# Kernel optimization log

Measured on AMD Instinct MI355X. Metric: run time of the kernel, lower is better.

## Reference

```python
import jax, jax.numpy as jnp
import numpy as np

IOU_THRESHOLD = 0.5
NEG_POS_RATIO = 3
FOCAL_ALPHA = 0.25
FOCAL_GAMMA = 2.0
LOC_LOSS_WEIGHT = 1.0
EPS = 1e-7


def _make_boxes(key, shape):
    # valid xyxy boxes in [0,1]
    k1, k2 = jax.random.split(key)
    xy1 = jax.random.uniform(k1, shape[:-1] + (2,)) * 0.8
    wh = jax.random.uniform(k2, shape[:-1] + (2,)) * 0.2 + 0.01
    return jnp.concatenate([xy1, xy1 + wh], axis=-1)


def setup_inputs() -> dict:
    key = jax.random.key(0)
    k1, k2, k3 = jax.random.split(key, 3)
    B, A, G = 16, 65536, 64
    bbox_pred = _make_boxes(k1, (B, A, 4))
    conf_pred = jax.random.normal(k2, (B, A), dtype=jnp.float32)
    gt_boxes = _make_boxes(k3, (B, G, 4))
    return {"bbox_pred": bbox_pred, "conf_pred": conf_pred, "gt_boxes": gt_boxes}


def box_iou(a, b):
    # a: [A,4], b: [G,4] xyxy -> [A,G]
    area_a = (a[:, 2] - a[:, 0]) * (a[:, 3] - a[:, 1])
    area_b = (b[:, 2] - b[:, 0]) * (b[:, 3] - b[:, 1])
    lt = jnp.maximum(a[:, None, :2], b[None, :, :2])
    rb = jnp.minimum(a[:, None, 2:], b[None, :, 2:])
    wh = jnp.clip(rb - lt, 0.0)
    inter = wh[..., 0] * wh[..., 1]
    return inter / (area_a[:, None] + area_b[None, :] - inter + EPS)


def diou_loss(pred, gt):
    # pred, gt: [N,4] xyxy -> [N]
    area_p = (pred[:, 2] - pred[:, 0]) * (pred[:, 3] - pred[:, 1])
    area_g = (gt[:, 2] - gt[:, 0]) * (gt[:, 3] - gt[:, 1])
    lt = jnp.maximum(pred[:, :2], gt[:, :2])
    rb = jnp.minimum(pred[:, 2:], gt[:, 2:])
    wh = jnp.clip(rb - lt, 0.0)
    inter = wh[:, 0] * wh[:, 1]
    iou = inter / (area_p + area_g - inter + EPS)
    cp = (pred[:, :2] + pred[:, 2:]) * 0.5
    cg = (gt[:, :2] + gt[:, 2:]) * 0.5
    center_d2 = jnp.sum((cp - cg) ** 2, axis=-1)
    elt = jnp.minimum(pred[:, :2], gt[:, :2])
    erb = jnp.maximum(pred[:, 2:], gt[:, 2:])
    diag2 = jnp.sum((erb - elt) ** 2, axis=-1) + EPS
    return 1.0 - iou + center_d2 / diag2


def focal_loss(logits, targets):
    # BCE-with-logits, stable
    ce = jnp.maximum(logits, 0.0) - logits * targets + jnp.log1p(jnp.exp(-jnp.abs(logits)))
    p = jax.nn.sigmoid(logits)
    p_t = jnp.clip(p * targets + (1 - p) * (1 - targets), EPS, 1.0 - EPS)
    focal_w = jax.lax.stop_gradient((1.0 - p_t) ** FOCAL_GAMMA)
    alpha_t = FOCAL_ALPHA * targets + (1 - FOCAL_ALPHA) * (1 - targets)
    return alpha_t * focal_w * ce


def _per_image(bb, cp, gt):
    A = cp.shape[0]
    ious = box_iou(bb, gt)                     # [A,G]
    best_gt_iou = ious.max(axis=1)             # [A]
    best_gt_idx = ious.argmax(axis=1)          # [A]
    best_anchor_idx = ious.argmax(axis=0)      # [G]
    pos = best_gt_iou > IOU_THRESHOLD
    pos = pos.at[best_anchor_idx].set(True)    # force best anchor per GT positive
    posf = pos.astype(cp.dtype)
    num_pos = posf.sum()

    matched_gt = gt[best_gt_idx]               # [A,4]
    loc = (diou_loss(bb, matched_gt) * posf).sum() * LOC_LOSS_WEIGHT

    fl = focal_loss(cp, posf)                  # [A]
    pos_sum = (fl * posf).sum()
    # hard-negative mining: descending sort of negative losses, keep top k
    neg_vals = jnp.where(pos, -1.0, fl)        # focal loss >= 0, so -1 sentinel
    sorted_neg = -jnp.sort(-neg_vals)
    num_neg = jnp.minimum(A - num_pos, num_pos * NEG_POS_RATIO)
    keep = jnp.arange(A) < num_neg
    neg_sum = jnp.where(keep, sorted_neg, 0.0).sum()
    conf = (pos_sum + neg_sum) / jnp.maximum(num_pos + num_neg, 1.0)
    return loc, conf, num_pos


def reference(bbox_pred, conf_pred, gt_boxes):
    loc, conf, npos = jax.vmap(_per_image)(bbox_pred, conf_pred, gt_boxes)
    total_pos = jnp.maximum(npos.sum(), 1.0)
    avg_loc = loc.sum() / total_pos
    avg_conf = conf.sum() / total_pos
    return avg_loc + avg_conf, avg_conf, avg_loc
```

## Files before the change

kernel.cpp:

```cpp
#include <hip/hip_runtime.h>
#include <stdint.h>

#define A_N 65536
#define B_N 16
#define G_N 64
#define FEPS 1e-7f

#define NBIN 2048
#define SHB  21
#define CAP  6144

__global__ __launch_bounds__(256) void dl_pass1(
    const float4* __restrict__ bbox, const float4* __restrict__ gt,
    float* __restrict__ posflag, uint8_t* __restrict__ best_idx,
    unsigned long long* __restrict__ gt_part, uint32_t* __restrict__ hist_zero,
    uint32_t* __restrict__ done_ctr) {
  const int img = blockIdx.y;
  const int bx  = blockIdx.x;
  const int t   = threadIdx.x;
  const int wave = t >> 6, lane = t & 63;
  const int a = bx * 256 + t;

  if (t < 16) hist_zero[(size_t)(img * 256 + bx) * 16 + t] = 0u;
  if (bx == 0 && img == 0 && t == 0) *done_ctr = 0u;

  __shared__ float4 sg[G_N];
  __shared__ float  sga[G_N];
  __shared__ unsigned long long spart[4][G_N];

  if (t < G_N) {
    float4 q0 = gt[img * G_N + t];
    sg[t] = q0;
    sga[t] = __fmul_rn(__fsub_rn(q0.z, q0.x), __fsub_rn(q0.w, q0.y));
  }
  __syncthreads();

  float4 p = bbox[img * A_N + a];
  float pa = __fmul_rn(__fsub_rn(p.z, p.x), __fsub_rn(p.w, p.y));

  float bi = 0.f, bd = 1.f; int bidx = 0; float posm = -1.f;
  uint32_t colkey = 0u;
  const int rotsrc = (lane + 1) & 63;
  const uint32_t lanecomp = 63u - (uint32_t)lane;

  int g = lane;
  #pragma unroll 4
  for (int j = 0; j < G_N; ++j) {
    float4 q = sg[g];
    float qa = sga[g];
    float ix1 = fmaxf(p.x, q.x), iy1 = fmaxf(p.y, q.y);
    float ix2 = fminf(p.z, q.z), iy2 = fminf(p.w, q.w);
    float iw = fmaxf(__fsub_rn(ix2, ix1), 0.f);
    float ih = fmaxf(__fsub_rn(iy2, iy1), 0.f);
    float inter = __fmul_rn(iw, ih);
    float den = __fadd_rn(__fsub_rn(__fadd_rn(pa, qa), inter), FEPS);
    if (inter * bd > bi * den) { bi = inter; bd = den; bidx = g; }
    posm = fmaxf(posm, __fmaf_rn(2.f, inter, -den));
    float ratio = inter * __builtin_amdgcn_rcpf(den);
    uint32_t key = (__float_as_uint(ratio) & 0xFFFFFFC0u) | lanecomp;
    if (key > colkey) colkey = key;
    colkey = __shfl(colkey, rotsrc);
    g = (g + 1) & 63;
  }

  posflag[img * A_N + a] = (posm > 0.f) ? 1.f : 0.f;
  best_idx[img * A_N + a] = (uint8_t)bidx;

  uint32_t winlane = 63u - (colkey & 63u);
  uint32_t ganchor = (uint32_t)(bx * 256 + wave * 64) + winlane;
  unsigned long long wkey = ((unsigned long long)(colkey & 0xFFFFFFC0u) << 32)
                          | (unsigned)~ganchor;
  spart[wave][lane] = wkey;
  __syncthreads();
  if (t < G_N) {
    unsigned long long m = spart[0][t];
    if (spart[1][t] > m) m = spart[1][t];
    if (spart[2][t] > m) m = spart[2][t];
    if (spart[3][t] > m) m = spart[3][t];
    gt_part[(((size_t)(img << 8) | bx) << 6) | t] = m;
  }
}

__global__ __launch_bounds__(64) void dl_force(const unsigned long long* __restrict__ gt_part,
                                               float* __restrict__ posflag) {
  const int p = blockIdx.x;
  const int img = p >> 6, g = p & 63;
  const int t = threadIdx.x;
  unsigned long long m = 0ull;
  #pragma unroll
  for (int j = 0; j < 4; ++j) {
    unsigned long long v = gt_part[(((size_t)(img << 8) | (t + j * 64)) << 6) | g];
    if (v > m) m = v;
  }
  for (int o = 32; o; o >>= 1) {
    unsigned long long other = __shfl_down(m, o);
    if (other > m) m = other;
  }
  if (t == 0) {
    uint32_t a = ~(uint32_t)(m & 0xFFFFFFFFull);
    posflag[(size_t)img * A_N + a] = 2.0f;
  }
}

__global__ __launch_bounds__(256) void dl_pass2(
    const float4* __restrict__ bbox, const float* __restrict__ conf,
    const float4* __restrict__ gt,
    const float* __restrict__ posflag, const uint8_t* __restrict__ best_idx,
    uint32_t* __restrict__ negkey,
    uint32_t* __restrict__ hist_cnt, float* __restrict__ hist_sum,
    float* __restrict__ part_loc, float* __restrict__ part_fl, float* __restrict__ part_np) {
  const int img = blockIdx.y;
  const int bx = blockIdx.x;
  const int a = bx * 256 + threadIdx.x;
  const int idx = img * A_N + a;

  __shared__ uint32_t hc[NBIN];
  __shared__ float    hs[NBIN];
  for (int i = threadIdx.x; i < NBIN; i += 256) { hc[i] = 0u; hs[i] = 0.f; }

  const bool pos = posflag[idx] > 0.5f;

  const float l = conf[idx];
  const float tt = pos ? 1.0f : 0.0f;
  float ce = fmaxf(l, 0.0f) - l * tt + log1pf(expf(-fabsf(l)));
  float pp = 1.0f / (1.0f + expf(-l));
  float pt = pp * tt + (1.0f - pp) * (1.0f - tt);
  pt = fminf(fmaxf(pt, FEPS), 1.0f - FEPS);
  float om = 1.0f - pt;
  float fl = (pos ? 0.25f : 0.75f) * om * om * ce;

  negkey[idx] = pos ? 0u : __float_as_uint(fl);

  float locv = 0.0f;
  if (pos) {
    float4 p = bbox[idx];
    float4 q = gt[img * G_N + best_idx[idx]];
    float ap = (p.z - p.x) * (p.w - p.y);
    float ag = (q.z - q.x) * (q.w - q.y);
    float ix1 = fmaxf(p.x, q.x), iy1 = fmaxf(p.y, q.y);
    float ix2 = fminf(p.z, q.z), iy2 = fminf(p.w, q.w);
    float iw = fmaxf(ix2 - ix1, 0.0f), ih = fmaxf(iy2 - iy1, 0.0f);
    float inter = iw * ih;
    float iou = inter / (ap + ag - inter + FEPS);
    float cpx = (p.x + p.z) * 0.5f, cpy = (p.y + p.w) * 0.5f;
    float cgx = (q.x + q.z) * 0.5f, cgy = (q.y + q.w) * 0.5f;
    float dx = cpx - cgx, dy = cpy - cgy;
    float cd2 = dx * dx + dy * dy;
    float ex1 = fminf(p.x, q.x), ey1 = fminf(p.y, q.y);
    float ex2 = fmaxf(p.z, q.z), ey2 = fmaxf(p.w, q.w);
    float ddx = ex2 - ex1, ddy = ey2 - ey1;
    float dg2 = ddx * ddx + ddy * ddy + FEPS;
    locv = 1.0f - iou + cd2 / dg2;
  }

  __syncthreads();
  if (!pos) {
    uint32_t kb = __float_as_uint(fl);
    atomicAdd(&hc[kb >> SHB], 1u);
    atomicAdd(&hs[kb >> SHB], fl);
  }

  float flp = pos ? fl : 0.0f;
  float np1 = pos ? 1.0f : 0.0f;
  for (int o = 32; o; o >>= 1) {
    locv += __shfl_down(locv, o);
    flp  += __shfl_down(flp, o);
    np1  += __shfl_down(np1, o);
  }
  __shared__ float sl[4], sf[4], sn[4];
  if ((threadIdx.x & 63) == 0) {
    int w = threadIdx.x >> 6;
    sl[w] = locv; sf[w] = flp; sn[w] = np1;
  }
  __syncthreads();
  for (int i = threadIdx.x; i < NBIN; i += 256) {
    uint32_t c = hc[i];
    if (c) {
      atomicAdd(&hist_cnt[img * NBIN + i], c);
      atomicAdd(&hist_sum[img * NBIN + i], hs[i]);
    }
  }
  if (threadIdx.x == 0) {
    const int pi = img * 256 + bx;
    part_loc[pi] = sl[0] + sl[1] + sl[2] + sl[3];
    part_fl[pi]  = sf[0] + sf[1] + sf[2] + sf[3];
    part_np[pi]  = sn[0] + sn[1] + sn[2] + sn[3];
  }
}

__global__ __launch_bounds__(1024) void dl_select(
    const uint32_t* __restrict__ negkey,
    const uint32_t* __restrict__ hist_cnt, const float* __restrict__ hist_sum,
    const float* __restrict__ part_loc, const float* __restrict__ part_fl,
    const float* __restrict__ part_np, float* __restrict__ acc,
    uint32_t* __restrict__ done_ctr, float* __restrict__ out) {
  const int img = blockIdx.x;
  const int t = threadIdx.x;
  const uint4* __restrict__ k4 = (const uint4*)(negkey + (size_t)img * A_N);
  const int N4 = A_N / 4;

  __shared__ uint32_t cnt[NBIN];
  __shared__ float    bsum[NBIN];
  __shared__ uint32_t cbuf[CAP];
  __shared__ float s3[3][4];
  __shared__ float redf[16];
  __shared__ int   redi[16];
  __shared__ float np_sh, psum_sh, loc_sh, sstar_sh, negsum_sh;
  __shared__ uint32_t bstar_sh, cstar_sh, ccnt_sh;

  for (int i = t; i < NBIN; i += 1024) {
    cnt[i]  = hist_cnt[img * NBIN + i];
    bsum[i] = hist_sum[img * NBIN + i];
  }

  float lv = 0.f, fv = 0.f, nv = 0.f;
  if (t < 256) {
    lv = part_loc[img * 256 + t];
    fv = part_fl[img * 256 + t];
    nv = part_np[img * 256 + t];
  }
  for (int o = 32; o; o >>= 1) {
    lv += __shfl_down(lv, o);
    fv += __shfl_down(fv, o);
    nv += __shfl_down(nv, o);
  }
  if (t < 256 && (t & 63) == 0) { s3[0][t >> 6] = lv; s3[1][t >> 6] = fv; s3[2][t >> 6] = nv; }
  __syncthreads();
  if (t == 0) {
    loc_sh  = s3[0][0] + s3[0][1] + s3[0][2] + s3[0][3];
    psum_sh = s3[1][0] + s3[1][1] + s3[1][2] + s3[1][3];
    np_sh   = s3[2][0] + s3[2][1] + s3[2][2] + s3[2][3];
    negsum_sh = 0.f;
  }
  __syncthreads();

  const int np = (int)(np_sh + 0.5f);
  const int k = min(A_N - np, 3 * np);

  if (k > 0) {
    if (t < 64) {
      const int CH = NBIN / 64;
      const int lob = NBIN - CH * (t + 1);
      uint32_t csum = 0;
      for (int b = lob; b < lob + CH; ++b) csum += cnt[b];
      uint32_t pre = csum;
      for (int o = 1; o < 64; o <<= 1) { uint32_t u = __shfl_up(pre, o); if (t >= o) pre += u; }
      uint32_t run = pre - csum;
      for (int b = lob + CH - 1; b >= lob; --b) {
        uint32_t c = cnt[b];
        if (run < (uint32_t)k && run + c >= (uint32_t)k) { bstar_sh = (uint32_t)b; cstar_sh = run; }
        run += c;
      }
    }
    __syncthreads();
    const int bstar = (int)bstar_sh;
    const uint32_t cstar = cstar_sh;
    const uint32_t cbin = cnt[bstar];
    const uint32_t r = (uint32_t)k - cstar;

    float s = 0.f;
    for (int i = t; i < NBIN; i += 1024) if (i > bstar) s += bsum[i];
    for (int o = 32; o; o >>= 1) s += __shfl_down(s, o);
    if ((t & 63) == 0) redf[t >> 6] = s;
    __syncthreads();
    if (t == 0) {
      float ss = 0.f;
      #pragma unroll
      for (int w = 0; w < 16; ++w) ss += redf[w];
      sstar_sh = ss;
    }
    __syncthreads();

    if (r == cbin) {
      if (t == 0) negsum_sh = sstar_sh + bsum[bstar];
    } else if (cbin <= (uint32_t)CAP) {
      if (t == 0) ccnt_sh = 0u;
      __syncthreads();
      for (int i = t; i < N4; i += 1024) {
        uint4 v = k4[i];
        if ((v.x >> SHB) == (uint32_t)bstar) cbuf[atomicAdd(&ccnt_sh, 1u)] = v.x;
        if ((v.y >> SHB) == (uint32_t)bstar) cbuf[atomicAdd(&ccnt_sh, 1u)] = v.y;
        if ((v.z >> SHB) == (uint32_t)bstar) cbuf[atomicAdd(&ccnt_sh, 1u)] = v.z;
        if ((v.w >> SHB) == (uint32_t)bstar) cbuf[atomicAdd(&ccnt_sh, 1u)] = v.w;
      }
      __syncthreads();
      if (t < 64) {
        const int n = (int)ccnt_sh;
        uint32_t lo = (uint32_t)bstar << SHB;
        uint32_t hi = ((uint32_t)bstar + 1u) << SHB;
        while (hi - lo > 1u) {
          uint32_t mid = lo + ((hi - lo) >> 1);
          int c = 0;
          for (int i = t; i < n; i += 64) c += (cbuf[i] >= mid) ? 1 : 0;
          for (int o = 32; o; o >>= 1) c += __shfl_down(c, o);
          c = __shfl(c, 0);
          if ((uint32_t)c >= r) lo = mid; else hi = mid;
        }
        float s2 = 0.f; int cg = 0;
        for (int i = t; i < n; i += 64) {
          uint32_t x = cbuf[i];
          if (x > lo) { s2 += __uint_as_float(x); cg++; }
        }
        for (int o = 32; o; o >>= 1) { s2 += __shfl_down(s2, o); cg += __shfl_down(cg, o); }
        if (t == 0) negsum_sh = sstar_sh + s2 + (float)(int)(r - (uint32_t)cg) * __uint_as_float(lo);
      }
    } else {
      uint32_t lo = (uint32_t)bstar << SHB;
      uint32_t hi = ((uint32_t)bstar + 1u) << SHB;
      while (hi - lo > 1u) {
        uint32_t mid = lo + ((hi - lo) >> 1);
        int c = 0;
        for (int i = t; i < N4; i += 1024) {
          uint4 v = k4[i];
          c += (v.x >= mid) + (v.y >= mid) + (v.z >= mid) + (v.w >= mid);
        }
        for (int o = 32; o; o >>= 1) c += __shfl_down(c, o);
        if ((t & 63) == 0) redi[t >> 6] = c;
        __syncthreads();
        c = 0;
        #pragma unroll
        for (int w = 0; w < 16; ++w) c += redi[w];
        __syncthreads();
        if (c >= k) lo = mid; else hi = mid;
      }
      float s2 = 0.f; int cg = 0;
      for (int i = t; i < N4; i += 1024) {
        uint4 v = k4[i];
        if (v.x > lo) { s2 += __uint_as_float(v.x); cg++; }
        if (v.y > lo) { s2 += __uint_as_float(v.y); cg++; }
        if (v.z > lo) { s2 += __uint_as_float(v.z); cg++; }
        if (v.w > lo) { s2 += __uint_as_float(v.w); cg++; }
      }
      for (int o = 32; o; o >>= 1) { s2 += __shfl_down(s2, o); cg += __shfl_down(cg, o); }
      if ((t & 63) == 0) { redf[t >> 6] = s2; redi[t >> 6] = cg; }
      __syncthreads();
      if (t == 0) {
        float ss = 0.f; int cc = 0;
        #pragma unroll
        for (int w = 0; w < 16; ++w) { ss += redf[w]; cc += redi[w]; }
        negsum_sh = ss + (float)(k - cc) * __uint_as_float(lo);
      }
    }
  }
  __syncthreads();
  if (t == 0) {
    acc[img] = loc_sh;
    acc[32 + img] = (float)np;
    acc[48 + img] = (psum_sh + negsum_sh) / fmaxf((float)(np + k), 1.0f);
    __threadfence();
    uint32_t old = atomicAdd(done_ctr, 1u);
    if (old == (uint32_t)(B_N - 1)) {
      __threadfence();
      float sl = 0.f, sc = 0.f, sn = 0.f;
      for (int i = 0; i < B_N; ++i) {
        sl += acc[i];
        sc += acc[48 + i];
        sn += acc[32 + i];
      }
      float tp = fmaxf(sn, 1.0f);
      float al = sl / tp;
      float ac = sc / tp;
      out[0] = al + ac;
      out[1] = ac;
      out[2] = al;
    }
  }
}

extern "C" void kernel_launch(void* const* d_in, const int* in_sizes, int n_in,
                              void* d_out, int out_size, void* d_ws, size_t ws_size,
                              hipStream_t stream) {
  (void)in_sizes; (void)n_in; (void)out_size; (void)ws_size;

  const float4* bbox = (const float4*)d_in[0];
  const float*  conf = (const float*)d_in[1];
  const float4* gt   = (const float4*)d_in[2];
  float* out = (float*)d_out;

  char* ws = (char*)d_ws;
  const size_t SZ = (size_t)B_N * A_N * 4;
  float*              posflag  = (float*)(ws);
  uint32_t*           negkey   = (uint32_t*)(ws + SZ);
  unsigned long long* gt_part  = (unsigned long long*)(ws + 2 * SZ);
  uint8_t*            best_idx = (uint8_t*)(ws + 2 * SZ + (size_t)B_N * 256 * G_N * 8);
  char* hb = ws + 2 * SZ + (size_t)B_N * 256 * G_N * 8 + (size_t)B_N * A_N;
  uint32_t* hist_cnt = (uint32_t*)(hb);
  float*    hist_sum = (float*)(hb + (size_t)B_N * NBIN * 4);
  char* tail = hb + 2 * (size_t)B_N * NBIN * 4;
  float* part_loc = (float*)(tail);
  float* part_fl  = (float*)(tail + 16384);
  float* part_np  = (float*)(tail + 32768);
  float* acc      = (float*)(tail + 49152);
  uint32_t* done_ctr = (uint32_t*)(tail + 49152 + 256);

  dl_pass1<<<dim3(A_N / 256, B_N), 256, 0, stream>>>(bbox, gt, posflag, best_idx, gt_part,
                                                     hist_cnt , done_ctr);
  dl_force<<<B_N * G_N, 64, 0, stream>>>(gt_part, posflag);
  dl_pass2<<<dim3(A_N / 256, B_N), 256, 0, stream>>>(bbox, conf, gt, posflag, best_idx,
                                                     negkey, hist_cnt, hist_sum,
                                                     part_loc, part_fl, part_np);
  dl_select<<<B_N, 1024, 0, stream>>>(negkey, hist_cnt, hist_sum,
                                      part_loc, part_fl, part_np, acc, done_ctr, out);
}
```

Measured before the change: 183.4 us.

## Fuse pass2 into pass1 and apply forced-positive corrections in select

Folds the focal loss, DIoU and negative-histogram work into the IoU pass, and removes the separate force and pass2 kernels along with the posflag buffer. The forced best-anchor-per-GT positives are now patched inside the select kernel: it reduces gt_part, zeroes those anchors' negkey entries, subtracts them from the histogram and adds their positive focal and DIoU terms. This saves two launches and a second full read of bbox, conf and posflag. In exchange, select gains serial fix-up work, and a separate init kernel is added to zero the histogram.

```diff
diff --git a/kernel.cpp b/kernel.cpp
--- a/kernel.cpp
+++ b/kernel.cpp
@@ -10,24 +10,63 @@
 #define SHB  21
 #define CAP  6144
 
+__device__ __forceinline__ float focal_one(float l, float tt) {
+  float ce = fmaxf(l, 0.0f) - l * tt + log1pf(expf(-fabsf(l)));
+  float pp = 1.0f / (1.0f + expf(-l));
+  float pt = pp * tt + (1.0f - pp) * (1.0f - tt);
+  pt = fminf(fmaxf(pt, FEPS), 1.0f - FEPS);
+  float om = 1.0f - pt;
+  float alpha = tt > 0.5f ? 0.25f : 0.75f;
+  return alpha * om * om * ce;
+}
+
+__device__ __forceinline__ float diou_one(float4 p, float4 q) {
+  float ap = (p.z - p.x) * (p.w - p.y);
+  float ag = (q.z - q.x) * (q.w - q.y);
+  float ix1 = fmaxf(p.x, q.x), iy1 = fmaxf(p.y, q.y);
+  float ix2 = fminf(p.z, q.z), iy2 = fminf(p.w, q.w);
+  float iw = fmaxf(ix2 - ix1, 0.0f), ih = fmaxf(iy2 - iy1, 0.0f);
+  float inter = iw * ih;
+  float iou = inter / (ap + ag - inter + FEPS);
+  float cpx = (p.x + p.z) * 0.5f, cpy = (p.y + p.w) * 0.5f;
+  float cgx = (q.x + q.z) * 0.5f, cgy = (q.y + q.w) * 0.5f;
+  float dx = cpx - cgx, dy = cpy - cgy;
+  float cd2 = dx * dx + dy * dy;
+  float ex1 = fminf(p.x, q.x), ey1 = fminf(p.y, q.y);
+  float ex2 = fmaxf(p.z, q.z), ey2 = fmaxf(p.w, q.w);
+  float ddx = ex2 - ex1, ddy = ey2 - ey1;
+  float dg2 = ddx * ddx + ddy * ddy + FEPS;
+  return 1.0f - iou + cd2 / dg2;
+}
+
+__global__ void dl_init(uint32_t* __restrict__ histz, uint32_t* __restrict__ done_ctr) {
+  int i = blockIdx.x * 1024 + threadIdx.x;
+  histz[i] = 0u;
+  if (i == 0) *done_ctr = 0u;
+}
+
 __global__ __launch_bounds__(256) void dl_pass1(
-    const float4* __restrict__ bbox, const float4* __restrict__ gt,
-    float* __restrict__ posflag, uint8_t* __restrict__ best_idx,
-    unsigned long long* __restrict__ gt_part, uint32_t* __restrict__ hist_zero,
-    uint32_t* __restrict__ done_ctr) {
+    const float4* __restrict__ bbox, const float* __restrict__ conf,
+    const float4* __restrict__ gt,
+    uint8_t* __restrict__ best_idx, uint32_t* __restrict__ negkey,
+    unsigned long long* __restrict__ gt_part,
+    uint32_t* __restrict__ hist_cnt, float* __restrict__ hist_sum,
+    float* __restrict__ part_loc, float* __restrict__ part_fl, float* __restrict__ part_np) {
   const int img = blockIdx.y;
   const int bx  = blockIdx.x;
   const int t   = threadIdx.x;
   const int wave = t >> 6, lane = t & 63;
   const int a = bx * 256 + t;
-
-  if (t < 16) hist_zero[(size_t)(img * 256 + bx) * 16 + t] = 0u;
-  if (bx == 0 && img == 0 && t == 0) *done_ctr = 0u;
+  const int idx = img * A_N + a;
 
   __shared__ float4 sg[G_N];
   __shared__ float  sga[G_N];
   __shared__ unsigned long long spart[4][G_N];
-
+  __shared__ uint32_t hc[NBIN];
+  __shared__ float    hs[NBIN];
+  __shared__ float sl[4], sf[4], sn[4];
+
+  for (int i = t; i < NBIN; i += 256) { hc[i] = 0u; hs[i] = 0.f; }
   if (t < G_N) {
     float4 q0 = gt[img * G_N + t];
     sg[t] = q0;
@@ -35,8 +74,9 @@
   }
   __syncthreads();
 
-  float4 p = bbox[img * A_N + a];
+  float4 p = bbox[idx];
   float pa = __fmul_rn(__fsub_rn(p.z, p.x), __fsub_rn(p.w, p.y));
+  float l = conf[idx];
 
   float bi = 0.f, bd = 1.f; int bidx = 0; float posm = -1.f;
   uint32_t colkey = 0u;
@@ -63,15 +103,42 @@
     g = (g + 1) & 63;
   }
 
-  posflag[img * A_N + a] = (posm > 0.f) ? 1.f : 0.f;
-  best_idx[img * A_N + a] = (uint8_t)bidx;
+  const bool pos = posm > 0.f;
+  best_idx[idx] = (uint8_t)bidx;
+
+  float fl = focal_one(l, pos ? 1.0f : 0.0f);
+  negkey[idx] = pos ? 0u : __float_as_uint(fl);
+  float locv = pos ? diou_one(p, sg[bidx]) : 0.0f;
+  if (!pos) {
+    uint32_t kb = __float_as_uint(fl);
+    atomicAdd(&hc[kb >> SHB], 1u);
+    atomicAdd(&hs[kb >> SHB], fl);
+  }
 
   uint32_t winlane = 63u - (colkey & 63u);
   uint32_t ganchor = (uint32_t)(bx * 256 + wave * 64) + winlane;
   unsigned long long wkey = ((unsigned long long)(colkey & 0xFFFFFFC0u) << 32)
                           | (unsigned)~ganchor;
   spart[wave][lane] = wkey;
-  __syncthreads();
+
+  float flp = pos ? fl : 0.0f;
+  float np1 = pos ? 1.0f : 0.0f;
+  float lv = locv;
+  for (int o = 32; o; o >>= 1) {
+    lv  += __shfl_down(lv, o);
+    flp += __shfl_down(flp, o);
+    np1 += __shfl_down(np1, o);
+  }
+  if (lane == 0) { sl[wave] = lv; sf[wave] = flp; sn[wave] = np1; }
+  __syncthreads();
+
+  for (int i = t; i < NBIN; i += 256) {
+    uint32_t c = hc[i];
+    if (c) {
+      atomicAdd(&hist_cnt[img * NBIN + i], c);
+      atomicAdd(&hist_sum[img * NBIN + i], hs[i]);
+    }
+  }
   if (t < G_N) {
     unsigned long long m = spart[0][t];
     if (spart[1][t] > m) m = spart[1][t];
@@ -79,108 +146,7 @@
     if (spart[3][t] > m) m = spart[3][t];
     gt_part[(((size_t)(img << 8) | bx) << 6) | t] = m;
   }
-}
-
-__global__ __launch_bounds__(64) void dl_force(const unsigned long long* __restrict__ gt_part,
-                                               float* __restrict__ posflag) {
-  const int p = blockIdx.x;
-  const int img = p >> 6, g = p & 63;
-  const int t = threadIdx.x;
-  unsigned long long m = 0ull;
-  #pragma unroll
-  for (int j = 0; j < 4; ++j) {
-    unsigned long long v = gt_part[(((size_t)(img << 8) | (t + j * 64)) << 6) | g];
-    if (v > m) m = v;
-  }
-  for (int o = 32; o; o >>= 1) {
-    unsigned long long other = __shfl_down(m, o);
-    if (other > m) m = other;
-  }
   if (t == 0) {
-    uint32_t a = ~(uint32_t)(m & 0xFFFFFFFFull);
-    posflag[(size_t)img * A_N + a] = 2.0f;
-  }
-}
-
-__global__ __launch_bounds__(256) void dl_pass2(
-    const float4* __restrict__ bbox, const float* __restrict__ conf,
-    const float4* __restrict__ gt,
-    const float* __restrict__ posflag, const uint8_t* __restrict__ best_idx,
-    uint32_t* __restrict__ negkey,
-    uint32_t* __restrict__ hist_cnt, float* __restrict__ hist_sum,
-    float* __restrict__ part_loc, float* __restrict__ part_fl, float* __restrict__ part_np) {
-  const int img = blockIdx.y;
-  const int bx = blockIdx.x;
-  const int a = bx * 256 + threadIdx.x;
-  const int idx = img * A_N + a;
-
-  __shared__ uint32_t hc[NBIN];
-  __shared__ float    hs[NBIN];
-  for (int i = threadIdx.x; i < NBIN; i += 256) { hc[i] = 0u; hs[i] = 0.f; }
-
-  const bool pos = posflag[idx] > 0.5f;
-
-  const float l = conf[idx];
-  const float tt = pos ? 1.0f : 0.0f;
-  float ce = fmaxf(l, 0.0f) - l * tt + log1pf(expf(-fabsf(l)));
-  float pp = 1.0f / (1.0f + expf(-l));
-  float pt = pp * tt + (1.0f - pp) * (1.0f - tt);
-  pt = fminf(fmaxf(pt, FEPS), 1.0f - FEPS);
-  float om = 1.0f - pt;
-  float fl = (pos ? 0.25f : 0.75f) * om * om * ce;
-
-  negkey[idx] = pos ? 0u : __float_as_uint(fl);
-
-  float locv = 0.0f;
-  if (pos) {
-    float4 p = bbox[idx];
-    float4 q = gt[img * G_N + best_idx[idx]];
-    float ap = (p.z - p.x) * (p.w - p.y);
-    float ag = (q.z - q.x) * (q.w - q.y);
-    float ix1 = fmaxf(p.x, q.x), iy1 = fmaxf(p.y, q.y);
-    float ix2 = fminf(p.z, q.z), iy2 = fminf(p.w, q.w);
-    float iw = fmaxf(ix2 - ix1, 0.0f), ih = fmaxf(iy2 - iy1, 0.0f);
-    float inter = iw * ih;
-    float iou = inter / (ap + ag - inter + FEPS);
-    float cpx = (p.x + p.z) * 0.5f, cpy = (p.y + p.w) * 0.5f;
-    float cgx = (q.x + q.z) * 0.5f, cgy = (q.y + q.w) * 0.5f;
-    float dx = cpx - cgx, dy = cpy - cgy;
-    float cd2 = dx * dx + dy * dy;
-    float ex1 = fminf(p.x, q.x), ey1 = fminf(p.y, q.y);
-    float ex2 = fmaxf(p.z, q.z), ey2 = fmaxf(p.w, q.w);
-    float ddx = ex2 - ex1, ddy = ey2 - ey1;
-    float dg2 = ddx * ddx + ddy * ddy + FEPS;
-    locv = 1.0f - iou + cd2 / dg2;
-  }
-
-  __syncthreads();
-  if (!pos) {
-    uint32_t kb = __float_as_uint(fl);
-    atomicAdd(&hc[kb >> SHB], 1u);
-    atomicAdd(&hs[kb >> SHB], fl);
-  }
-
-  float flp = pos ? fl : 0.0f;
-  float np1 = pos ? 1.0f : 0.0f;
-  for (int o = 32; o; o >>= 1) {
-    locv += __shfl_down(locv, o);
-    flp  += __shfl_down(flp, o);
-    np1  += __shfl_down(np1, o);
-  }
-  __shared__ float sl[4], sf[4], sn[4];
-  if ((threadIdx.x & 63) == 0) {
-    int w = threadIdx.x >> 6;
-    sl[w] = locv; sf[w] = flp; sn[w] = np1;
-  }
-  __syncthreads();
-  for (int i = threadIdx.x; i < NBIN; i += 256) {
-    uint32_t c = hc[i];
-    if (c) {
-      atomicAdd(&hist_cnt[img * NBIN + i], c);
-      atomicAdd(&hist_sum[img * NBIN + i], hs[i]);
-    }
-  }
-  if (threadIdx.x == 0) {
     const int pi = img * 256 + bx;
     part_loc[pi] = sl[0] + sl[1] + sl[2] + sl[3];
     part_fl[pi]  = sf[0] + sf[1] + sf[2] + sf[3];
@@ -189,30 +155,45 @@
 }
 
 __global__ __launch_bounds__(1024) void dl_select(
-    const uint32_t* __restrict__ negkey,
+    uint32_t* negkey,
+    const unsigned long long* __restrict__ gt_part,
     const uint32_t* __restrict__ hist_cnt, const float* __restrict__ hist_sum,
     const float* __restrict__ part_loc, const float* __restrict__ part_fl,
-    const float* __restrict__ part_np, float* __restrict__ acc,
-    uint32_t* __restrict__ done_ctr, float* __restrict__ out) {
+    const float* __restrict__ part_np,
+    const float4* __restrict__ bbox, const float* __restrict__ conf,
+    const float4* __restrict__ gt, const uint8_t* __restrict__ best_idx,
+    float* __restrict__ acc, uint32_t* __restrict__ done_ctr, float* __restrict__ out) {
   const int img = blockIdx.x;
   const int t = threadIdx.x;
-  const uint4* __restrict__ k4 = (const uint4*)(negkey + (size_t)img * A_N);
+  uint32_t* negk = negkey + (size_t)img * A_N;
+  const uint4* k4 = (const uint4*)negk;
   const int N4 = A_N / 4;
 
   __shared__ uint32_t cnt[NBIN];
   __shared__ float    bsum[NBIN];
   __shared__ uint32_t cbuf[CAP];
+  __shared__ unsigned long long gred[16][G_N];
   __shared__ float s3[3][4];
   __shared__ float redf[16];
   __shared__ int   redi[16];
   __shared__ float np_sh, psum_sh, loc_sh, sstar_sh, negsum_sh;
+  __shared__ float fix_l, fix_f, fix_n;
   __shared__ uint32_t bstar_sh, cstar_sh, ccnt_sh;
 
   for (int i = t; i < NBIN; i += 1024) {
     cnt[i]  = hist_cnt[img * NBIN + i];
     bsum[i] = hist_sum[img * NBIN + i];
   }
-
+  {
+    const int g = t & 63, ch = t >> 6;
+    unsigned long long m = 0ull;
+    #pragma unroll 4
+    for (int j = 0; j < 16; ++j) {
+      unsigned long long v = gt_part[(((size_t)(img << 8) | (ch * 16 + j)) << 6) | g];
+      if (v > m) m = v;
+    }
+    gred[ch][g] = m;
+  }
   float lv = 0.f, fv = 0.f, nv = 0.f;
   if (t < 256) {
     lv = part_loc[img * 256 + t];
@@ -226,10 +207,38 @@
   }
   if (t < 256 && (t & 63) == 0) { s3[0][t >> 6] = lv; s3[1][t >> 6] = fv; s3[2][t >> 6] = nv; }
   __syncthreads();
+
+  if (t < 64) {
+    unsigned long long m = gred[0][t];
+    #pragma unroll
+    for (int c = 1; c < 16; ++c) if (gred[c][t] > m) m = gred[c][t];
+    uint32_t a = ~(uint32_t)(m & 0xFFFFFFFFull);
+    uint32_t old = atomicExch(&negk[a], 0u);
+    float dl = 0.f, df = 0.f, dn = 0.f;
+    if (old != 0u) {
+      dn = 1.f;
+      float fln = __uint_as_float(old);
+      uint32_t bin = old >> SHB;
+      atomicSub(&cnt[bin], 1u);
+      atomicAdd(&bsum[bin], -fln);
+      const int ai = img * A_N + (int)a;
+      df = focal_one(conf[ai], 1.0f);
+      dl = diou_one(bbox[ai], gt[img * G_N + best_idx[ai]]);
+    }
+    for (int o = 32; o; o >>= 1) {
+      dl += __shfl_down(dl, o);
+      df += __shfl_down(df, o);
+      dn += __shfl_down(dn, o);
+    }
+    if (t == 0) { fix_l = dl; fix_f = df; fix_n = dn; }
+  }
+  __threadfence();
+  __syncthreads();
+
   if (t == 0) {
-    loc_sh  = s3[0][0] + s3[0][1] + s3[0][2] + s3[0][3];
-    psum_sh = s3[1][0] + s3[1][1] + s3[1][2] + s3[1][3];
-    np_sh   = s3[2][0] + s3[2][1] + s3[2][2] + s3[2][3];
+    loc_sh  = s3[0][0] + s3[0][1] + s3[0][2] + s3[0][3] + fix_l;
+    psum_sh = s3[1][0] + s3[1][1] + s3[1][2] + s3[1][3] + fix_f;
+    np_sh   = s3[2][0] + s3[2][1] + s3[2][2] + s3[2][3] + fix_n;
     negsum_sh = 0.f;
   }
   __syncthreads();
@@ -378,12 +387,10 @@
   float* out = (float*)d_out;
 
   char* ws = (char*)d_ws;
-  const size_t SZ = (size_t)B_N * A_N * 4;
-  float*              posflag  = (float*)(ws);
-  uint32_t*           negkey   = (uint32_t*)(ws + SZ);
-  unsigned long long* gt_part  = (unsigned long long*)(ws + 2 * SZ);
-  uint8_t*            best_idx = (uint8_t*)(ws + 2 * SZ + (size_t)B_N * 256 * G_N * 8);
-  char* hb = ws + 2 * SZ + (size_t)B_N * 256 * G_N * 8 + (size_t)B_N * A_N;
+  uint32_t*           negkey   = (uint32_t*)(ws);
+  unsigned long long* gt_part  = (unsigned long long*)(ws + (4u << 20));
+  uint8_t*            best_idx = (uint8_t*)(ws + (6u << 20));
+  char* hb = ws + (7u << 20);
   uint32_t* hist_cnt = (uint32_t*)(hb);
   float*    hist_sum = (float*)(hb + (size_t)B_N * NBIN * 4);
   char* tail = hb + 2 * (size_t)B_N * NBIN * 4;
@@ -393,12 +400,11 @@
   float* acc      = (float*)(tail + 49152);
   uint32_t* done_ctr = (uint32_t*)(tail + 49152 + 256);
 
-  dl_pass1<<<dim3(A_N / 256, B_N), 256, 0, stream>>>(bbox, gt, posflag, best_idx, gt_part,
-                                                     hist_cnt , done_ctr);
-  dl_force<<<B_N * G_N, 64, 0, stream>>>(gt_part, posflag);
-  dl_pass2<<<dim3(A_N / 256, B_N), 256, 0, stream>>>(bbox, conf, gt, posflag, best_idx,
-                                                     negkey, hist_cnt, hist_sum,
+  dl_init<<<64, 1024, 0, stream>>>(hist_cnt , done_ctr);
+  dl_pass1<<<dim3(A_N / 256, B_N), 256, 0, stream>>>(bbox, conf, gt, best_idx, negkey,
+                                                     gt_part, hist_cnt, hist_sum,
                                                      part_loc, part_fl, part_np);
-  dl_select<<<B_N, 1024, 0, stream>>>(negkey, hist_cnt, hist_sum,
-                                      part_loc, part_fl, part_np, acc, done_ctr, out);
-}
+  dl_select<<<B_N, 1024, 0, stream>>>(negkey, gt_part, hist_cnt, hist_sum,
+                                      part_loc, part_fl, part_np,
+                                      bbox, conf, gt, best_idx, acc, done_ctr, out);
+}
```

Result: faster. 172.7 us (-5.9%).
